# Performance work log

Hardware: AMD Instinct MI355X
Metric: run time of the kernel (lower is better)

Reference implementation:

```python
import jax, jax.numpy as jnp
import numpy as np

H = 8   # num_key_value_heads
G = 4   # num_query_heads // num_key_value_heads
HQ = H * G  # 32 query heads


def setup_inputs() -> dict:
    key = jax.random.key(0)
    k0, k1, k2, k3 = jax.random.split(key, 4)
    B, N, D = 2, 2048, 2048
    s = 1.0 / np.sqrt(D)
    x = jax.random.normal(k0, (B, N, D), jnp.float32)
    Wq = jax.random.normal(k1, (D, D), jnp.float32) * s
    Wkv = jax.random.normal(k2, (D, 2 * D // G), jnp.float32) * s
    Wp = jax.random.normal(k3, (D, D), jnp.float32) * s
    bp = jnp.zeros((D,), jnp.float32)
    return {"x": x, "Wq": Wq, "Wkv": Wkv, "Wp": Wp, "bp": bp}


def reference(x, Wq, Wkv, Wp, bp):
    B, N, D = x.shape
    C = D // (H * G)  # head dim
    scale = float(np.sqrt(HQ))  # module scales by sqrt(num_query_heads)
    q = (x @ Wq) / scale                     # [B, N, D]
    kv = x @ Wkv                             # [B, N, 2*H*C]
    k, v = jnp.split(kv, 2, axis=-1)         # each [B, N, H*C]
    # q: b n (h g c) -> b g h n c
    q = q.reshape(B, N, H, G, C).transpose(0, 3, 2, 1, 4)
    # k, v: b s (h c) -> b h s c
    k = k.reshape(B, N, H, C).transpose(0, 2, 1, 3)
    v = v.reshape(B, N, H, C).transpose(0, 2, 1, 3)
    sim = jnp.einsum('bghnc,bhsc->bghns', q, k)
    attn = jax.nn.softmax(sim, axis=-1)
    o = jnp.einsum('bghns,bhsc->bghnc', attn, v)
    # b g h n c -> b n (h g c)
    o = o.transpose(0, 3, 2, 1, 4).reshape(B, N, D)
    return o @ Wp + bp
```

## Files before the change

### kernel.cpp

```cpp
#include <hip/hip_runtime.h>
#include <hip/hip_bf16.h>
#include <math.h>

typedef __attribute__((ext_vector_type(8))) __bf16 bf16x8;
typedef __attribute__((ext_vector_type(4))) float f32x4;
typedef __attribute__((ext_vector_type(16))) float f32x16;
typedef __attribute__((ext_vector_type(2))) unsigned u32x2;

#define MFMA16(a, b, c) __builtin_amdgcn_mfma_f32_16x16x32_bf16((a), (b), (c), 0, 0, 0)
#define MFMA32(a, b, c) __builtin_amdgcn_mfma_f32_32x32x16_bf16((a), (b), (c), 0, 0, 0)

#define GLOAD_LDS(g, l)                                                                     \
  __builtin_amdgcn_global_load_lds((const __attribute__((address_space(1))) unsigned int*)(g), \
                                   (__attribute__((address_space(3))) unsigned int*)(l), 16, 0, 0)

static constexpr int Bb  = 2;
static constexpr int Nn  = 2048;
static constexpr int Dd  = 2048;
static constexpr int Hh  = 8;
static constexpr int Gg  = 4;
static constexpr int Cc  = 64;
static constexpr int KVW = 1024;

__device__ __forceinline__ unsigned short f2bf(float f) {
  unsigned int u = __float_as_uint(f);
  u += 0x7FFFu + ((u >> 16) & 1u);
  return (unsigned short)(u >> 16);
}

__device__ __forceinline__ float xhalf_sum(float v) {
  u32x2 r = __builtin_amdgcn_permlane32_swap(__float_as_uint(v), __float_as_uint(v), false, false);
  return __uint_as_float(r.x) + __uint_as_float(r.y);
}

__global__ void xconv(const float* __restrict__ x, unsigned short* __restrict__ xb, int n4) {
  int i = blockIdx.x * blockDim.x + threadIdx.x;
  const int stride = gridDim.x * blockDim.x;
  for (; i < n4; i += stride) {
    float4 v = ((const float4*)x)[i];
    ushort4 o;
    o.x = f2bf(v.x); o.y = f2bf(v.y); o.z = f2bf(v.z); o.w = f2bf(v.w);
    ((ushort4*)xb)[i] = o;
  }
}

__global__ void wconv(const float* __restrict__ W, unsigned short* __restrict__ Wt,
                      int K, int N, float scale) {
  __shared__ float t[32][33];
  const int n0 = blockIdx.x * 32, k0 = blockIdx.y * 32;
  for (int i = threadIdx.x; i < 1024; i += blockDim.x) {
    int r = i >> 5, c = i & 31;
    t[r][c] = W[(size_t)(k0 + r) * N + n0 + c];
  }
  __syncthreads();
  for (int i = threadIdx.x; i < 1024; i += blockDim.x) {
    int r = i >> 5, c = i & 31;
    Wt[(size_t)(n0 + r) * K + k0 + c] = f2bf(t[c][r] * scale);
  }
}

__global__ void vtrans(const unsigned short* __restrict__ kvb, unsigned short* __restrict__ vT) {
  __shared__ unsigned short t[64][72];
  const int s0 = blockIdx.x * 64;
  const int b = blockIdx.y >> 3, h = blockIdx.y & 7;
  const unsigned short* src = kvb + ((size_t)b * Nn + s0) * KVW + Hh * Cc + h * Cc;
  for (int i = threadIdx.x; i < 4096; i += blockDim.x) {
    int s = i >> 6, c = i & 63;
    t[s][c] = src[(size_t)s * KVW + c];
  }
  __syncthreads();
  unsigned short* dst = vT + (size_t)(b * Hh + h) * Cc * Nn + s0;
  for (int i = threadIdx.x; i < 4096; i += blockDim.x) {
    int c = i >> 6, s = i & 63;
    dst[(size_t)c * Nn + s] = t[s][c];
  }
}

template <bool OUTF32>
__global__ __launch_bounds__(256, 2)
void gemm_bt(const unsigned short* __restrict__ A, const unsigned short* __restrict__ Bt,
             unsigned short* __restrict__ Cb, float* __restrict__ Cf,
             const float* __restrict__ bias, int M, int N, int K) {
  __shared__ unsigned short As[2][128 * 64];
  __shared__ unsigned short Bs[2][128 * 64];
  const int tid = threadIdx.x;
  const int wid = tid >> 6, lane = tid & 63;
  const size_t m0 = (size_t)blockIdx.x * 128;
  const size_t n0 = (size_t)blockIdx.y * 128;
  const int nk = K >> 6;

  const int sub = lane >> 3, slot = lane & 7;
  const int gslot = slot ^ sub;
  const unsigned short* gA[4];
  const unsigned short* gB[4];
#pragma unroll
  for (int i = 0; i < 4; ++i) {
    const int c = wid * 4 + i;
    gA[i] = A + (m0 + c * 8 + sub) * (size_t)K + gslot * 8;
    gB[i] = Bt + (n0 + c * 8 + sub) * (size_t)K + gslot * 8;
  }

  auto stage = [&](int bi) {
#pragma unroll
    for (int i = 0; i < 4; ++i) {
      const int c = wid * 4 + i;
      GLOAD_LDS(gA[i], &As[bi][c * 512]);
      GLOAD_LDS(gB[i], &Bs[bi][c * 512]);
      gA[i] += 64;
      gB[i] += 64;
    }
  };

  const int wr = wid >> 1, wc = wid & 1;
  const int lrow = lane & 15, lg = lane >> 4;
  int aoff[4][2], boff[4][2];
#pragma unroll
  for (int mt = 0; mt < 4; ++mt)
#pragma unroll
    for (int kc = 0; kc < 2; ++kc) {
      const int ra = wr * 64 + mt * 16 + lrow;
      const int rb = wc * 64 + mt * 16 + lrow;
      const int sl = (((kc << 2) + lg) ^ (lrow & 7)) << 4;
      aoff[mt][kc] = ra * 128 + sl;
      boff[mt][kc] = rb * 128 + sl;
    }

  const f32x4 zero = {0.f, 0.f, 0.f, 0.f};
  f32x4 acc[4][4];
#pragma unroll
  for (int i = 0; i < 4; ++i)
#pragma unroll
    for (int j = 0; j < 4; ++j) acc[i][j] = zero;

  auto compute = [&](int bi) {
    const char* Ab = (const char*)&As[bi][0];
    const char* Bb2 = (const char*)&Bs[bi][0];
#pragma unroll
    for (int kc = 0; kc < 2; ++kc) {
      bf16x8 af[4], bfr[4];
#pragma unroll
      for (int mt = 0; mt < 4; ++mt) af[mt] = *(const bf16x8*)(Ab + aoff[mt][kc]);
#pragma unroll
      for (int nt = 0; nt < 4; ++nt) bfr[nt] = *(const bf16x8*)(Bb2 + boff[nt][kc]);
#pragma unroll
      for (int mt = 0; mt < 4; ++mt)
#pragma unroll
        for (int nt = 0; nt < 4; ++nt) acc[mt][nt] = MFMA16(af[mt], bfr[nt], acc[mt][nt]);
    }
  };

  stage(0);
  __syncthreads();
  for (int kt = 0; kt < nk; kt += 2) {
    stage(1);
    compute(0);
    __syncthreads();
    if (kt + 2 < nk) stage(0);
    compute(1);
    __syncthreads();
  }

#pragma unroll
  for (int mt = 0; mt < 4; ++mt)
#pragma unroll
    for (int nt = 0; nt < 4; ++nt) {
      const size_t col = n0 + wc * 64 + nt * 16 + lrow;
#pragma unroll
      for (int i = 0; i < 4; ++i) {
        const size_t r = m0 + wr * 64 + mt * 16 + lg * 4 + i;
        if constexpr (OUTF32)
          Cf[r * N + col] = acc[mt][nt][i] + bias[col];
        else
          Cb[r * N + col] = f2bf(acc[mt][nt][i]);
      }
    }
}

__global__ __launch_bounds__(512, 4)
void attn_kernel(const unsigned short* __restrict__ qb, const unsigned short* __restrict__ kvb,
                 const unsigned short* __restrict__ vT, unsigned short* __restrict__ ob) {
  __shared__ unsigned short Ks[2][4096];
  __shared__ unsigned short Vs[2][4096];
  const int tid = threadIdx.x;
  const int wid = tid >> 6, lane = tid & 63;
  const int r31 = lane & 31, hi = lane >> 5, r7 = r31 & 7;
  const int q0 = blockIdx.x * 256 + wid * 32;
  const int bhg = blockIdx.y;
  const int b = bhg >> 5, h = (bhg >> 2) & 7, g = bhg & 3;

  const unsigned short* kptr = kvb + (size_t)b * Nn * KVW + h * Cc;
  const unsigned short* vptr = vT + (size_t)(b * Hh + h) * Cc * Nn;

  const int sub = lane >> 3, slot = lane & 7;
  const int gslot = slot ^ sub;
  const unsigned short* gk = kptr + (size_t)(wid * 8 + sub) * KVW + gslot * 8;
  const unsigned short* gv = vptr + (size_t)(wid * 8 + sub) * Nn + gslot * 8;

  bf16x8 qf[4];
  {
    const unsigned short* qrow =
        qb + ((size_t)b * Nn + q0 + r31) * Dd + h * (Gg * Cc) + g * Cc + hi * 8;
#pragma unroll
    for (int ks = 0; ks < 4; ++ks) qf[ks] = *(const bf16x8*)(qrow + ks * 16);
  }

  int off[4];
#pragma unroll
  for (int ks = 0; ks < 4; ++ks) off[ks] = r31 * 128 + (((2 * ks + hi) ^ r7) << 4);

  f32x16 O0 = (f32x16)0.0f, O1 = (f32x16)0.0f;
  float L_ = 0.0f;

  auto stage = [&](int bi) {
    GLOAD_LDS(gk, &Ks[bi][wid * 512]);
    GLOAD_LDS(gv, &Vs[bi][wid * 512]);
    gk += (size_t)64 * KVW;
    gv += 64;
  };

  auto compute = [&](const unsigned short* Kb_, const unsigned short* Vb_) {
    const char* Kb = (const char*)Kb_;
    const char* Vb = (const char*)Vb_;
    f32x16 S0 = (f32x16)0.0f, S1 = (f32x16)0.0f;
    __builtin_amdgcn_s_setprio(1);
#pragma unroll
    for (int ks = 0; ks < 4; ++ks) {
      bf16x8 k0 = *(const bf16x8*)(Kb + off[ks]);
      bf16x8 k1 = *(const bf16x8*)(Kb + off[ks] + 4096);
      S0 = MFMA32(k0, qf[ks], S0);
      S1 = MFMA32(k1, qf[ks], S1);
    }
    __builtin_amdgcn_s_setprio(0);
    float rs = 0.0f;
    unsigned pk[16];
#pragma unroll
    for (int kt2 = 0; kt2 < 2; ++kt2)
#pragma unroll
      for (int blk = 0; blk < 4; ++blk)
#pragma unroll
        for (int m = 0; m < 2; ++m) {
          float pa = __expf(kt2 ? S1[4 * blk + 2 * m] : S0[4 * blk + 2 * m]);
          float pb = __expf(kt2 ? S1[4 * blk + 2 * m + 1] : S0[4 * blk + 2 * m + 1]);
          rs += pa + pb;
          float2 f2; f2.x = pa; f2.y = pb;
          __hip_bfloat162 hpk = __float22bfloat162_rn(f2);
          pk[kt2 * 8 + blk * 2 + m] = *reinterpret_cast<unsigned*>(&hpk);
        }
    L_ += xhalf_sum(rs);
    __builtin_amdgcn_s_setprio(1);
#pragma unroll
    for (int vs = 0; vs < 4; ++vs) {
      const int base = (vs >> 1) * 8 + (vs & 1) * 4;
      u32x2 rA = __builtin_amdgcn_permlane32_swap(pk[base + 0], pk[base + 2], false, false);
      u32x2 rB = __builtin_amdgcn_permlane32_swap(pk[base + 1], pk[base + 3], false, false);
      union { unsigned u[4]; bf16x8 v; } pf;
      pf.u[0] = rA.x; pf.u[1] = rB.x; pf.u[2] = rA.y; pf.u[3] = rB.y;
      bf16x8 v0 = *(const bf16x8*)(Vb + off[vs]);
      bf16x8 v1 = *(const bf16x8*)(Vb + off[vs] + 4096);
      O0 = MFMA32(pf.v, v0, O0);
      O1 = MFMA32(pf.v, v1, O1);
    }
    __builtin_amdgcn_s_setprio(0);
  };

  stage(0);
  __syncthreads();
  for (int t = 0; t < Nn / 64; t += 2) {
    stage(1);
    compute(Ks[0], Vs[0]);
    __syncthreads();
    if (t + 2 < Nn / 64) stage(0);
    compute(Ks[1], Vs[1]);
    __syncthreads();
  }

  float Linv = 1.0f / L_;
  const size_t orow_base = (size_t)b * Nn + q0;
  const int ocol = h * (Gg * Cc) + g * Cc;
#pragma unroll
  for (int r = 0; r < 16; ++r) {
    const int q_r = (r & 3) + 8 * (r >> 2) + 4 * hi;
    float li = __shfl(Linv, q_r);
    const size_t basep = (orow_base + q_r) * Dd + ocol;
    ob[basep + r31] = f2bf(O0[r] * li);
    ob[basep + 32 + r31] = f2bf(O1[r] * li);
  }
}

extern "C" void kernel_launch(void* const* d_in, const int* in_sizes, int n_in,
                              void* d_out, int out_size, void* d_ws, size_t ws_size,
                              hipStream_t stream) {
  const float* x   = (const float*)d_in[0];
  const float* Wq  = (const float*)d_in[1];
  const float* Wkv = (const float*)d_in[2];
  const float* Wp  = (const float*)d_in[3];
  const float* bp  = (const float*)d_in[4];
  float* out = (float*)d_out;

  char* ws = (char*)d_ws;
  size_t off = 0;
  auto alloc = [&](size_t bytes) {
    char* p = ws + off;
    off += (bytes + 255) & ~(size_t)255;
    return p;
  };
  unsigned short* xb   = (unsigned short*)alloc((size_t)Bb * Nn * Dd * 2);
  unsigned short* Wqt  = (unsigned short*)alloc((size_t)Dd * Dd * 2);
  unsigned short* Wkvt = (unsigned short*)alloc((size_t)KVW * Dd * 2);
  unsigned short* Wpt  = (unsigned short*)alloc((size_t)Dd * Dd * 2);
  unsigned short* qbf  = (unsigned short*)alloc((size_t)Bb * Nn * Dd * 2);
  unsigned short* kvb  = (unsigned short*)alloc((size_t)Bb * Nn * KVW * 2);
  unsigned short* vT   = (unsigned short*)alloc((size_t)Bb * Hh * Cc * Nn * 2);
  unsigned short* ob   = xb;

  const int M = Bb * Nn;
  const float qscale = 0.17677669529663687f;

  xconv<<<2048, 256, 0, stream>>>(x, xb, (Bb * Nn * Dd) / 4);
  wconv<<<dim3(Dd / 32, Dd / 32), 256, 0, stream>>>(Wq, Wqt, Dd, Dd, qscale);
  wconv<<<dim3(KVW / 32, Dd / 32), 256, 0, stream>>>(Wkv, Wkvt, Dd, KVW, 1.0f);
  wconv<<<dim3(Dd / 32, Dd / 32), 256, 0, stream>>>(Wp, Wpt, Dd, Dd, 1.0f);

  gemm_bt<false><<<dim3(M / 128, Dd / 128), 256, 0, stream>>>(xb, Wqt, qbf, nullptr, nullptr, M, Dd, Dd);
  gemm_bt<false><<<dim3(M / 128, KVW / 128), 256, 0, stream>>>(xb, Wkvt, kvb, nullptr, nullptr, M, KVW, Dd);
  vtrans<<<dim3(Nn / 64, Bb * Hh), 256, 0, stream>>>(kvb, vT);
  attn_kernel<<<dim3(Nn / 256, Bb * Hh * Gg), 512, 0, stream>>>(qbf, kvb, vT, ob);
  gemm_bt<true><<<dim3(M / 128, Dd / 128), 256, 0, stream>>>(ob, Wpt, nullptr, out, bp, M, Dd, Dd);
}
```

Baseline: 244.4 us.

## Switch GEMM to 32x32 MFMA tiles and compute softmax denominator via MFMA

The GEMM kernel moves from a 4x4 grid of 16x16x32 MFMAs to a 2x2 grid of 32x32x16 MFMAs per wave. This cuts the number of LDS fragment reads per k-step and uses the larger matrix instruction. In the attention kernel, the softmax row sum is now accumulated by an extra MFMA of the bf16 probabilities against a ones vector, replacing the scalar adds and cross-half permlane reduction. The trade-off is 50% more MFMA work in the PV phase and a denominator computed from bf16-rounded probabilities.

```diff
diff --git a/kernel.cpp b/kernel.cpp
--- a/kernel.cpp
+++ b/kernel.cpp
@@ -7,7 +7,6 @@
 typedef __attribute__((ext_vector_type(16))) float f32x16;
 typedef __attribute__((ext_vector_type(2))) unsigned u32x2;
 
-#define MFMA16(a, b, c) __builtin_amdgcn_mfma_f32_16x16x32_bf16((a), (b), (c), 0, 0, 0)
 #define MFMA32(a, b, c) __builtin_amdgcn_mfma_f32_32x32x16_bf16((a), (b), (c), 0, 0, 0)
 
 #define GLOAD_LDS(g, l)                                                                     \
@@ -26,11 +25,6 @@
   unsigned int u = __float_as_uint(f);
   u += 0x7FFFu + ((u >> 16) & 1u);
   return (unsigned short)(u >> 16);
-}
-
-__device__ __forceinline__ float xhalf_sum(float v) {
-  u32x2 r = __builtin_amdgcn_permlane32_swap(__float_as_uint(v), __float_as_uint(v), false, false);
-  return __uint_as_float(r.x) + __uint_as_float(r.y);
 }
 
 __global__ void xconv(const float* __restrict__ x, unsigned short* __restrict__ xb, int n4) {
@@ -112,40 +106,33 @@
   };
 
   const int wr = wid >> 1, wc = wid & 1;
-  const int lrow = lane & 15, lg = lane >> 4;
-  int aoff[4][2], boff[4][2];
-#pragma unroll
-  for (int mt = 0; mt < 4; ++mt)
-#pragma unroll
-    for (int kc = 0; kc < 2; ++kc) {
-      const int ra = wr * 64 + mt * 16 + lrow;
-      const int rb = wc * 64 + mt * 16 + lrow;
-      const int sl = (((kc << 2) + lg) ^ (lrow & 7)) << 4;
-      aoff[mt][kc] = ra * 128 + sl;
-      boff[mt][kc] = rb * 128 + sl;
-    }
-
-  const f32x4 zero = {0.f, 0.f, 0.f, 0.f};
-  f32x4 acc[4][4];
-#pragma unroll
-  for (int i = 0; i < 4; ++i)
-#pragma unroll
-    for (int j = 0; j < 4; ++j) acc[i][j] = zero;
+  const int r31 = lane & 31, hi = lane >> 5, r7 = r31 & 7;
+  int aoff[2][4], boff[2][4];
+#pragma unroll
+  for (int t2 = 0; t2 < 2; ++t2)
+#pragma unroll
+    for (int ks = 0; ks < 4; ++ks) {
+      const int sl = (((ks << 1) + hi) ^ r7) << 4;
+      aoff[t2][ks] = (wr * 64 + t2 * 32 + r31) * 128 + sl;
+      boff[t2][ks] = (wc * 64 + t2 * 32 + r31) * 128 + sl;
+    }
+
+  f32x16 acc00 = (f32x16)0.0f, acc01 = (f32x16)0.0f;
+  f32x16 acc10 = (f32x16)0.0f, acc11 = (f32x16)0.0f;
 
   auto compute = [&](int bi) {
     const char* Ab = (const char*)&As[bi][0];
     const char* Bb2 = (const char*)&Bs[bi][0];
 #pragma unroll
-    for (int kc = 0; kc < 2; ++kc) {
-      bf16x8 af[4], bfr[4];
-#pragma unroll
-      for (int mt = 0; mt < 4; ++mt) af[mt] = *(const bf16x8*)(Ab + aoff[mt][kc]);
-#pragma unroll
-      for (int nt = 0; nt < 4; ++nt) bfr[nt] = *(const bf16x8*)(Bb2 + boff[nt][kc]);
-#pragma unroll
-      for (int mt = 0; mt < 4; ++mt)
-#pragma unroll
-        for (int nt = 0; nt < 4; ++nt) acc[mt][nt] = MFMA16(af[mt], bfr[nt], acc[mt][nt]);
+    for (int ks = 0; ks < 4; ++ks) {
+      bf16x8 a0 = *(const bf16x8*)(Ab + aoff[0][ks]);
+      bf16x8 a1 = *(const bf16x8*)(Ab + aoff[1][ks]);
+      bf16x8 b0 = *(const bf16x8*)(Bb2 + boff[0][ks]);
+      bf16x8 b1 = *(const bf16x8*)(Bb2 + boff[1][ks]);
+      acc00 = MFMA32(a0, b0, acc00);
+      acc01 = MFMA32(a0, b1, acc01);
+      acc10 = MFMA32(a1, b0, acc10);
+      acc11 = MFMA32(a1, b1, acc11);
     }
   };
 
@@ -161,17 +148,18 @@
   }
 
 #pragma unroll
-  for (int mt = 0; mt < 4; ++mt)
-#pragma unroll
-    for (int nt = 0; nt < 4; ++nt) {
-      const size_t col = n0 + wc * 64 + nt * 16 + lrow;
-#pragma unroll
-      for (int i = 0; i < 4; ++i) {
-        const size_t r = m0 + wr * 64 + mt * 16 + lg * 4 + i;
+  for (int mt2 = 0; mt2 < 2; ++mt2)
+#pragma unroll
+    for (int nt2 = 0; nt2 < 2; ++nt2) {
+      const f32x16& a = mt2 == 0 ? (nt2 == 0 ? acc00 : acc01) : (nt2 == 0 ? acc10 : acc11);
+      const size_t col = n0 + wc * 64 + nt2 * 32 + r31;
+#pragma unroll
+      for (int r = 0; r < 16; ++r) {
+        const size_t row = m0 + wr * 64 + mt2 * 32 + (r & 3) + 8 * (r >> 2) + 4 * hi;
         if constexpr (OUTF32)
-          Cf[r * N + col] = acc[mt][nt][i] + bias[col];
+          Cf[row * N + col] = a[r] + bias[col];
         else
-          Cb[r * N + col] = f2bf(acc[mt][nt][i]);
+          Cb[row * N + col] = f2bf(a[r]);
       }
     }
 }
@@ -204,12 +192,14 @@
     for (int ks = 0; ks < 4; ++ks) qf[ks] = *(const bf16x8*)(qrow + ks * 16);
   }
 
+  union { unsigned u[4]; bf16x8 v; } ones;
+  ones.u[0] = ones.u[1] = ones.u[2] = ones.u[3] = 0x3F803F80u;
+
   int off[4];
 #pragma unroll
   for (int ks = 0; ks < 4; ++ks) off[ks] = r31 * 128 + (((2 * ks + hi) ^ r7) << 4);
 
-  f32x16 O0 = (f32x16)0.0f, O1 = (f32x16)0.0f;
-  float L_ = 0.0f;
+  f32x16 O0 = (f32x16)0.0f, O1 = (f32x16)0.0f, Lacc = (f32x16)0.0f;
 
   auto stage = [&](int bi) {
     GLOAD_LDS(gk, &Ks[bi][wid * 512]);
@@ -231,7 +221,6 @@
       S1 = MFMA32(k1, qf[ks], S1);
     }
     __builtin_amdgcn_s_setprio(0);
-    float rs = 0.0f;
     unsigned pk[16];
 #pragma unroll
     for (int kt2 = 0; kt2 < 2; ++kt2)
@@ -241,12 +230,10 @@
         for (int m = 0; m < 2; ++m) {
           float pa = __expf(kt2 ? S1[4 * blk + 2 * m] : S0[4 * blk + 2 * m]);
           float pb = __expf(kt2 ? S1[4 * blk + 2 * m + 1] : S0[4 * blk + 2 * m + 1]);
-          rs += pa + pb;
           float2 f2; f2.x = pa; f2.y = pb;
           __hip_bfloat162 hpk = __float22bfloat162_rn(f2);
           pk[kt2 * 8 + blk * 2 + m] = *reinterpret_cast<unsigned*>(&hpk);
         }
-    L_ += xhalf_sum(rs);
     __builtin_amdgcn_s_setprio(1);
 #pragma unroll
     for (int vs = 0; vs < 4; ++vs) {
@@ -259,6 +246,7 @@
       bf16x8 v1 = *(const bf16x8*)(Vb + off[vs] + 4096);
       O0 = MFMA32(pf.v, v0, O0);
       O1 = MFMA32(pf.v, v1, O1);
+      Lacc = MFMA32(pf.v, ones.v, Lacc);
     }
     __builtin_amdgcn_s_setprio(0);
   };
@@ -274,13 +262,12 @@
     __syncthreads();
   }
 
-  float Linv = 1.0f / L_;
   const size_t orow_base = (size_t)b * Nn + q0;
   const int ocol = h * (Gg * Cc) + g * Cc;
 #pragma unroll
   for (int r = 0; r < 16; ++r) {
     const int q_r = (r & 3) + 8 * (r >> 2) + 4 * hi;
-    float li = __shfl(Linv, q_r);
+    const float li = 1.0f / Lacc[r];
     const size_t basep = (orow_base + q_r) * Dd + ocol;
     ob[basep + r31] = f2bf(O0[r] * li);
     ob[basep + 32 + r31] = f2bf(O1[r] * li);
```

After: 246.9 us. No clear change (+1.0%).
